# Optimization experiments

Measured on AMD Instinct MI355X. Metric: run time of the kernel, lower is better.

The kernel has to match this reference:

```python
import jax, jax.numpy as jnp
import numpy as np

B, C1, C2, H, W = 8, 256, 512, 56, 56

def setup_inputs() -> dict:
    key = jax.random.key(0)
    k1, k2, k3, k4, k5 = jax.random.split(key, 5)
    return {
        "x1": jax.random.normal(k1, (B, C1, H, W), dtype=jnp.float32),
        "x2": jax.random.normal(k2, (B, C2, H, W), dtype=jnp.float32),
        "W_proj": jax.random.normal(k3, (C1, C2), dtype=jnp.float32) * (1.0 / np.sqrt(C2)),
        "b_proj": jax.random.normal(k4, (C1,), dtype=jnp.float32) * 0.01,
        "gamma": jax.random.normal(k5, (1,), dtype=jnp.float32) * 0.1,
    }

def reference(x1, x2, W_proj, b_proj, gamma):
    b, c, h, w = x1.shape
    n = h * w
    # 1x1 conv projection C2 -> C1
    x2p = jnp.einsum('oc,bchw->bohw', W_proj, x2) + b_proj[None, :, None, None]
    query = x1.reshape(b, c, n).transpose(0, 2, 1)   # [B, N, C]
    key_ = x2p.reshape(b, c, n)                      # [B, C, N]
    value = x2p.reshape(b, c, n).transpose(0, 2, 1)  # [B, N, C]
    energy = jnp.einsum('bnc,bcm->bnm', query, key_)  # [B, N, N]
    # inverted-energy softmax: max - energy, then softmax over last dim
    energy_new = jnp.max(energy, axis=-1, keepdims=True) - energy
    attention = jax.nn.softmax(energy_new, axis=-1)
    out = jnp.einsum('bnm,bmc->bnc', attention, value)  # [B, N, C]
    out = out.transpose(0, 2, 1).reshape(b, c, h, w)
    return gamma[0] * out + x1
```

## Files before the change

kernel.cpp:

```cpp
#include <hip/hip_runtime.h>
#include <hip/hip_bf16.h>

#define C1 256
#define C2 512
#define NSP 3136
#define NT 98

typedef __attribute__((ext_vector_type(8))) short bf16x8;
typedef __attribute__((ext_vector_type(4))) float f32x4;

__device__ __forceinline__ ushort f2b(float f) {
  __hip_bfloat16 h = __float2bfloat16(f);
  return *reinterpret_cast<ushort*>(&h);
}
__device__ __forceinline__ float b2f(ushort u) {
  union { unsigned int i; float f; } v; v.i = ((unsigned int)u) << 16; return v.f;
}
__device__ __forceinline__ void gload16(const ushort* g, ushort* l) {
  __builtin_amdgcn_global_load_lds(
      (const __attribute__((address_space(1))) void*)g,
      (__attribute__((address_space(3))) void*)l, 16, 0, 0);
}
__device__ __forceinline__ void block_bar() {
  asm volatile("" ::: "memory");
  __builtin_amdgcn_s_barrier();
  asm volatile("" ::: "memory");
}

__global__ __launch_bounds__(256) void k_wtf(const float* __restrict__ W,
                                             ushort* __restrict__ Wf) {
  int ot = blockIdx.x;
  int tid = threadIdx.x;
  int lane = tid & 63, l15 = lane & 15, g = (lane >> 4) & 3;
  int cc0 = (tid >> 6) * 4;
  const float* src = W + (size_t)(ot * 16 + l15) * C2 + g * 8;
#pragma unroll
  for (int k = 0; k < 4; k++) {
    int cc = cc0 + k;
    float4 u0 = *reinterpret_cast<const float4*>(src + cc * 32);
    float4 u1 = *reinterpret_cast<const float4*>(src + cc * 32 + 4);
    bf16x8 v;
    v[0] = (short)f2b(u0.x); v[1] = (short)f2b(u0.y);
    v[2] = (short)f2b(u0.z); v[3] = (short)f2b(u0.w);
    v[4] = (short)f2b(u1.x); v[5] = (short)f2b(u1.y);
    v[6] = (short)f2b(u1.z); v[7] = (short)f2b(u1.w);
    *reinterpret_cast<bf16x8*>(Wf + ((size_t)(ot * 16 + cc)) * 512 + lane * 8) = v;
  }
}

__global__ __launch_bounds__(256) void k_x1t(const float* __restrict__ x1,
                                             ushort* __restrict__ x1t) {
  __shared__ float t[32][33];
  int b = blockIdx.z;
  int n0 = blockIdx.x * 32;
  int c0 = blockIdx.y * 32;
  int tid = threadIdx.x;
  int r = tid >> 3, q = (tid & 7) * 4;
  const float* src = x1 + ((size_t)b * C1 + (c0 + r)) * NSP + n0 + q;
  float4 v = *reinterpret_cast<const float4*>(src);
  t[r][q] = v.x; t[r][q + 1] = v.y; t[r][q + 2] = v.z; t[r][q + 3] = v.w;
  __syncthreads();
  ushort4 o;
  o.x = f2b(t[q + 0][r]); o.y = f2b(t[q + 1][r]);
  o.z = f2b(t[q + 2][r]); o.w = f2b(t[q + 3][r]);
  *reinterpret_cast<ushort4*>(x1t + ((size_t)b * NSP + n0 + r) * C1 + c0 + q) = o;
}

__global__ __launch_bounds__(256) void k_x2f(const float* __restrict__ x2,
                                             ushort* __restrict__ x2f) {
  __shared__ float t[32][33];
  int b = blockIdx.z;
  int n0 = blockIdx.x * 32;
  int cc = blockIdx.y;
  int c0 = cc * 32;
  int tid = threadIdx.x;
  int r = tid >> 3, q = (tid & 7) * 4;
  const float* src = x2 + ((size_t)b * C2 + (c0 + r)) * NSP + n0 + q;
  float4 v = *reinterpret_cast<const float4*>(src);
  t[r][q] = v.x; t[r][q + 1] = v.y; t[r][q + 2] = v.z; t[r][q + 3] = v.w;
  __syncthreads();
  int l15 = tid & 15, g = (tid >> 4) & 3, sub = tid >> 6;
  int ntl = sub & 1, ih = sub >> 1;
  int nl = ntl * 16 + l15;
  int cl = g * 8 + ih * 4;
  ushort4 o;
  o.x = f2b(t[cl + 0][nl]); o.y = f2b(t[cl + 1][nl]);
  o.z = f2b(t[cl + 2][nl]); o.w = f2b(t[cl + 3][nl]);
  int nt16 = (n0 >> 4) + ntl;
  *reinterpret_cast<ushort4*>(
      x2f + (((size_t)b * 196 + nt16) * 16 + cc) * 512 + (size_t)(tid & 63) * 8 + ih * 4) = o;
}

__global__ __launch_bounds__(256) void k_proj(const ushort* __restrict__ Wf,
    const ushort* __restrict__ x2f, const float* __restrict__ bias,
    ushort* __restrict__ Kf, ushort* __restrict__ Vf) {
  __shared__ __align__(16) ushort WL[2][8][512];
  __shared__ __align__(16) ushort XL[2][4][512];
  int bid = blockIdx.x;
  int b = bid & 7;
  int tq = bid >> 3;
  int oh = tq & 1;
  int nt = tq >> 1;
  int tid = threadIdx.x;
  int w = tid >> 6, lane = tid & 63, l15 = lane & 15, g = lane >> 4;
  int wq = w >> 1, wn = w & 1;
  int ot0 = oh * 8;
  int nt0 = nt * 4;

  auto stage = [&](int buf, int cc) {
#pragma unroll
    for (int j = 0; j < 3; j++) {
      int chunk = w * 3 + j;
      if (chunk < 8) {
        gload16(Wf + ((size_t)(ot0 + chunk) * 16 + cc) * 512 + lane * 8,
                &WL[buf][chunk][0]);
      } else {
        gload16(x2f + (((size_t)b * 196 + nt0 + (chunk - 8)) * 16 + cc) * 512 + lane * 8,
                &XL[buf][chunk - 8][0]);
      }
    }
  };

  f32x4 zero = {0.f, 0.f, 0.f, 0.f};
  f32x4 acc[4][2];
#pragma unroll
  for (int a = 0; a < 4; a++)
#pragma unroll
    for (int v = 0; v < 2; v++) acc[a][v] = zero;

  stage(0, 0);
  __syncthreads();

  for (int cc = 0; cc < 16; ++cc) {
    int cur = cc & 1;
    if (cc < 15) stage(cur ^ 1, cc + 1);
    bf16x8 A[4], Bf[2];
#pragma unroll
    for (int a = 0; a < 4; a++)
      A[a] = *reinterpret_cast<const bf16x8*>(&WL[cur][wq * 4 + a][lane * 8]);
#pragma unroll
    for (int v = 0; v < 2; v++)
      Bf[v] = *reinterpret_cast<const bf16x8*>(&XL[cur][wn * 2 + v][lane * 8]);
#pragma unroll
    for (int a = 0; a < 4; a++)
#pragma unroll
      for (int v = 0; v < 2; v++)
        acc[a][v] = __builtin_amdgcn_mfma_f32_16x16x32_bf16(A[a], Bf[v], acc[a][v], 0, 0, 0);
    __syncthreads();
  }

  int obase = oh * 128 + wq * 64;
  float4 bias4[4];
#pragma unroll
  for (int a = 0; a < 4; a++)
    bias4[a] = *reinterpret_cast<const float4*>(&bias[obase + a * 16 + g * 4]);

  int gk = (g & 1) * 4;
#pragma unroll
  for (int a = 0; a < 4; a++) {
    int laneK = (((2 * a + (g >> 1)) & 3) << 4) | l15;
    size_t oK = (size_t)(oh * 4 + wq * 2 + (a >> 1));
#pragma unroll
    for (int v = 0; v < 2; v++) {
      int nK = nt * 4 + wn * 2 + v;
      ushort4 st;
      st.x = f2b(acc[a][v][0] + bias4[a].x);
      st.y = f2b(acc[a][v][1] + bias4[a].y);
      st.z = f2b(acc[a][v][2] + bias4[a].z);
      st.w = f2b(acc[a][v][3] + bias4[a].w);
      *reinterpret_cast<ushort4*>(
          Kf + ((((size_t)b * 196 + nK) * 8 + oK) * 64 + laneK) * 8 + gk) = st;
    }
  }
  int nV = nt * 2 + wn;
#pragma unroll
  for (int v = 0; v < 2; v++) {
    int gv = ((v * 2 + (l15 >> 3)) & 3) << 4;
    int iV = l15 & 7;
#pragma unroll
    for (int a = 0; a < 4; a++) {
      int cs = oh * 8 + wq * 4 + a;
      size_t basev = ((((size_t)b * 98 + nV) * 16 + cs) * 64 + gv) * 8 + iV;
      const float* bp4 = reinterpret_cast<const float*>(&bias4[a]);
#pragma unroll
      for (int r = 0; r < 4; r++)
        Vf[basev + (size_t)(g * 4 + r) * 8] = f2b(acc[a][v][r] + bp4[r]);
    }
  }
}

template<int SPLIT>
__global__ __launch_bounds__(256, 3) void k_attn(
    const ushort* __restrict__ x1t, const ushort* __restrict__ Kf,
    const ushort* __restrict__ Vf, const float* __restrict__ x1,
    const float* __restrict__ gamma, float* __restrict__ out,
    ushort* __restrict__ Po, float* __restrict__ Mv, float* __restrict__ Lv) {
  __shared__ __align__(16) ushort Kt[2][8192];
  __shared__ __align__(16) ushort Vt[8192];
  __shared__ __align__(16) ushort Plds[4][16][36];
  int bid = blockIdx.x;
  int b = bid & 7;
  int qt = SPLIT ? (bid >> 4) : (bid >> 3);
  int h = SPLIT ? ((bid >> 3) & 1) : 0;
  int t0 = h * 49;
  int t1 = SPLIT ? (t0 + 49) : NT;
  int tid = threadIdx.x;
  int w = tid >> 6;
  int lane = tid & 63;
  int l15 = lane & 15;
  int g = lane >> 4;
  int n0 = qt * 64 + w * 16;

  bf16x8 qf[8];
  const ushort* qb = x1t + ((size_t)b * NSP + n0 + l15) * C1 + g * 8;
#pragma unroll
  for (int cc = 0; cc < 8; cc++)
    qf[cc] = *reinterpret_cast<const bf16x8*>(qb + cc * 32);

  f32x4 zero = {0.f, 0.f, 0.f, 0.f};
  f32x4 O[16];
#pragma unroll
  for (int i = 0; i < 16; i++) O[i] = zero;
  f32x4 O17 = zero;
  float M[4];
#pragma unroll
  for (int r = 0; r < 4; r++) M[r] = -3.0e38f;
  bf16x8 onesf;
#pragma unroll
  for (int i = 0; i < 8; i++) onesf[i] = (short)0x3F80;

  const ushort* kg = Kf + (size_t)b * 196 * 8 * 512;
  const ushort* vg = Vf + (size_t)b * 98 * 16 * 512;
  int soff = w * 2048;

  {
    const ushort* ks = kg + (size_t)t0 * 8192 + soff + lane * 8;
#pragma unroll
    for (int j = 0; j < 4; ++j) gload16(ks + j * 512, &Kt[0][soff] + j * 512);
  }
  asm volatile("s_waitcnt vmcnt(0)" ::: "memory");
  block_bar();

  int cur = 0;
  for (int t = t0; t < t1; ++t) {
    {
      const ushort* vs = vg + (size_t)t * 8192 + soff + lane * 8;
#pragma unroll
      for (int j = 0; j < 4; ++j) gload16(vs + j * 512, &Vt[soff] + j * 512);
    }
    asm volatile("" ::: "memory");
    if (t + 1 < t1) {
      const ushort* ks = kg + (size_t)(t + 1) * 8192 + soff + lane * 8;
#pragma unroll
      for (int j = 0; j < 4; ++j) gload16(ks + j * 512, &Kt[cur ^ 1][soff] + j * 512);
    }
    asm volatile("" ::: "memory");

    f32x4 s0a = zero, s0b = zero, s1a = zero, s1b = zero;
    const ushort* kb = &Kt[cur][0];
    __builtin_amdgcn_s_setprio(1);
#pragma unroll
    for (int cc = 0; cc < 8; cc += 2) {
      bf16x8 k00 = *reinterpret_cast<const bf16x8*>(kb + ((size_t)cc * 64 + lane) * 8);
      bf16x8 k10 = *reinterpret_cast<const bf16x8*>(kb + ((size_t)(8 + cc) * 64 + lane) * 8);
      bf16x8 k01 = *reinterpret_cast<const bf16x8*>(kb + ((size_t)(cc + 1) * 64 + lane) * 8);
      bf16x8 k11 = *reinterpret_cast<const bf16x8*>(kb + ((size_t)(9 + cc) * 64 + lane) * 8);
      s0a = __builtin_amdgcn_mfma_f32_16x16x32_bf16(qf[cc], k00, s0a, 0, 0, 0);
      s1a = __builtin_amdgcn_mfma_f32_16x16x32_bf16(qf[cc], k10, s1a, 0, 0, 0);
      s0b = __builtin_amdgcn_mfma_f32_16x16x32_bf16(qf[cc + 1], k01, s0b, 0, 0, 0);
      s1b = __builtin_amdgcn_mfma_f32_16x16x32_bf16(qf[cc + 1], k11, s1b, 0, 0, 0);
    }
    __builtin_amdgcn_s_setprio(0);

    float a0[4], a1[4], tmax[4];
#pragma unroll
    for (int r = 0; r < 4; r++) {
      a0[r] = -(s0a[r] + s0b[r]);
      a1[r] = -(s1a[r] + s1b[r]);
      float mx = fmaxf(a0[r], a1[r]);
      mx = fmaxf(mx, __shfl_xor(mx, 1));
      mx = fmaxf(mx, __shfl_xor(mx, 2));
      mx = fmaxf(mx, __shfl_xor(mx, 4));
      mx = fmaxf(mx, __shfl_xor(mx, 8));
      tmax[r] = mx;
    }
    float d01 = fmaxf(tmax[0] - M[0], tmax[1] - M[1]);
    float d23 = fmaxf(tmax[2] - M[2], tmax[3] - M[3]);
    if (__any(fmaxf(d01, d23) > 3.0f)) {
      float scv[4];
#pragma unroll
      for (int r = 0; r < 4; r++) {
        float nm = fmaxf(M[r], tmax[r]);
        scv[r] = __expf(M[r] - nm);
        M[r] = nm;
      }
#pragma unroll
      for (int i = 0; i < 16; i++) {
#pragma unroll
        for (int r = 0; r < 4; r++) O[i][r] *= scv[r];
      }
#pragma unroll
      for (int r = 0; r < 4; r++) O17[r] *= scv[r];
    }
#pragma unroll
    for (int r = 0; r < 4; r++) {
      float p0 = __expf(a0[r] - M[r]);
      float p1 = __expf(a1[r] - M[r]);
      Plds[w][g * 4 + r][l15] = f2b(p0);
      Plds[w][g * 4 + r][16 + l15] = f2b(p1);
    }

    if (t + 1 < t1) { asm volatile("s_waitcnt vmcnt(4)" ::: "memory"); }
    else            { asm volatile("s_waitcnt vmcnt(0)" ::: "memory"); }
    block_bar();

    bf16x8 pf = *reinterpret_cast<const bf16x8*>(&Plds[w][l15][g * 8]);
    __builtin_amdgcn_s_setprio(1);
#pragma unroll
    for (int cs = 0; cs < 16; ++cs) {
      bf16x8 vf = *reinterpret_cast<const bf16x8*>(&Vt[0] + ((size_t)cs * 64 + lane) * 8);
      O[cs] = __builtin_amdgcn_mfma_f32_16x16x32_bf16(pf, vf, O[cs], 0, 0, 0);
    }
    O17 = __builtin_amdgcn_mfma_f32_16x16x32_bf16(pf, onesf, O17, 0, 0, 0);
    __builtin_amdgcn_s_setprio(0);

    asm volatile("s_waitcnt vmcnt(0)" ::: "memory");
    block_bar();
    cur ^= 1;
  }

  if (SPLIT) {
    int pb = bid;
    int nloc = w * 16 + g * 4;
#pragma unroll
    for (int cs = 0; cs < 16; cs++) {
      int c = cs * 16 + l15;
      ushort4 st;
      st.x = f2b(O[cs][0]); st.y = f2b(O[cs][1]);
      st.z = f2b(O[cs][2]); st.w = f2b(O[cs][3]);
      *reinterpret_cast<ushort4*>(Po + ((size_t)pb * 256 + c) * 64 + nloc) = st;
    }
    if (l15 == 0) {
#pragma unroll
      for (int r = 0; r < 4; r++) {
        Mv[(size_t)pb * 64 + nloc + r] = M[r];
        Lv[(size_t)pb * 64 + nloc + r] = O17[r];
      }
    }
  } else {
    float gm = gamma[0];
    float rl[4];
#pragma unroll
    for (int r = 0; r < 4; r++) rl[r] = gm / O17[r];
    size_t ob = (size_t)b * C1 * NSP + n0 + (size_t)g * 4;
#pragma unroll
    for (int cs = 0; cs < 16; cs++) {
      size_t idx = ob + (size_t)(cs * 16 + l15) * NSP;
      float4 x4 = *reinterpret_cast<const float4*>(&x1[idx]);
      float4 o4;
      o4.x = O[cs][0] * rl[0] + x4.x;
      o4.y = O[cs][1] * rl[1] + x4.y;
      o4.z = O[cs][2] * rl[2] + x4.z;
      o4.w = O[cs][3] * rl[3] + x4.w;
      *reinterpret_cast<float4*>(&out[idx]) = o4;
    }
  }
}

__global__ __launch_bounds__(256) void k_comb(
    const ushort* __restrict__ Po, const float* __restrict__ Mv,
    const float* __restrict__ Lv, const float* __restrict__ x1,
    const float* __restrict__ gamma, float* __restrict__ out) {
  int bid = blockIdx.x;
  int b = bid & 7;
  int qt = bid >> 3;
  int tid = threadIdx.x;
  int n = tid & 63;
  int c0 = (tid >> 6) * 64;
  int pb0 = qt * 16 + b;
  int pb1 = qt * 16 + 8 + b;
  int n0 = qt * 64;
  float M0 = Mv[(size_t)pb0 * 64 + n], M1 = Mv[(size_t)pb1 * 64 + n];
  float L0 = Lv[(size_t)pb0 * 64 + n], L1 = Lv[(size_t)pb1 * 64 + n];
  float Ms = fmaxf(M0, M1);
  float w0 = __expf(M0 - Ms), w1 = __expf(M1 - Ms);
  float rl = gamma[0] / (w0 * L0 + w1 * L1);
  const ushort* p0 = Po + (size_t)pb0 * 16384 + n;
  const ushort* p1 = Po + (size_t)pb1 * 16384 + n;
#pragma unroll 4
  for (int c = c0; c < c0 + 64; ++c) {
    float o0 = b2f(p0[(size_t)c * 64]);
    float o1 = b2f(p1[(size_t)c * 64]);
    size_t idx = ((size_t)b * C1 + c) * NSP + n0 + n;
    out[idx] = (w0 * o0 + w1 * o1) * rl + x1[idx];
  }
}

extern "C" void kernel_launch(void* const* d_in, const int* in_sizes, int n_in,
                              void* d_out, int out_size, void* d_ws, size_t ws_size,
                              hipStream_t stream) {
  const float* x1 = (const float*)d_in[0];
  const float* x2 = (const float*)d_in[1];
  const float* W = (const float*)d_in[2];
  const float* bp = (const float*)d_in[3];
  const float* gamma = (const float*)d_in[4];
  float* out = (float*)d_out;

  char* ws = (char*)d_ws;
  ushort* Wf = (ushort*)(ws + 0);
  ushort* x1t = (ushort*)(ws + 524288);
  ushort* Kf = (ushort*)(ws + 13369344);
  ushort* Vf = (ushort*)(ws + 26214400);
  ushort* Po = (ushort*)(ws + 39059456);
  float* Mv = (float*)(ws + 64749568);
  float* Lv = (float*)(ws + 64950272);
  ushort* x2f = (ushort*)d_out;

  k_wtf<<<dim3(16), dim3(256), 0, stream>>>(W, Wf);
  k_x1t<<<dim3(98, 8, 8), dim3(256), 0, stream>>>(x1, x1t);
  k_x2f<<<dim3(98, 16, 8), dim3(256), 0, stream>>>(x2, x2f);
  k_proj<<<dim3(784), dim3(256), 0, stream>>>(Wf, x2f, bp, Kf, Vf);

  if (ws_size >= 65150976ULL) {
    k_attn<1><<<dim3(784), dim3(256), 0, stream>>>(x1t, Kf, Vf, x1, gamma, out,
                                                   Po, Mv, Lv);
    k_comb<<<dim3(392), dim3(256), 0, stream>>>(Po, Mv, Lv, x1, gamma, out);
  } else {
    k_attn<0><<<dim3(392), dim3(256), 0, stream>>>(x1t, Kf, Vf, x1, gamma, out,
                                                   Po, Mv, Lv);
  }
}
```

Baseline: 255.6 us.

## Add stream-K cooperative attention kernel with in-kernel grid-sync combine

Adds a cooperative attention kernel that splits the 8x49 query-tile by 98 key-tile work evenly across 768 blocks (51 tiles each, stream-K style). Each block crosses query-tile boundaries, spilling partial O/M/L for tiles it does not own, then does a grid-wide sync and the owning block merges the partials and writes the output. This removes the separate combine kernel launch and the load imbalance of fixed 784/392-block splits. In exchange it needs cooperative launch with all 768 blocks co-resident, and it falls back to the old path if that launch fails. It also shrinks the workspace offsets and adds an lgkmcnt wait before reading P from LDS.

```diff
diff --git a/kernel.cpp b/kernel.cpp
--- a/kernel.cpp
+++ b/kernel.cpp
@@ -1,5 +1,8 @@
 #include <hip/hip_runtime.h>
 #include <hip/hip_bf16.h>
+#include <hip/hip_cooperative_groups.h>
+
+namespace cg = cooperative_groups;
 
 #define C1 256
 #define C2 512
@@ -189,6 +192,256 @@
   }
 }
 
+__global__ __launch_bounds__(256, 3) void k_attn_q(
+    const ushort* __restrict__ x1t, const ushort* __restrict__ Kf,
+    const ushort* __restrict__ Vf, const float* __restrict__ x1,
+    const float* __restrict__ gamma, float* __restrict__ out,
+    ushort* __restrict__ Po, float* __restrict__ Mv, float* __restrict__ Lv) {
+  __shared__ __align__(16) ushort Kt[2][8192];
+  __shared__ __align__(16) ushort Vt[8192];
+  __shared__ __align__(16) ushort Plds[4][16][36];
+  int bid = blockIdx.x;
+  int x = bid & 7;
+  int j = bid >> 3;
+  int s = 51 * j; if (s > 4802) s = 4802;
+  int e = 51 * j + 51; if (e > 4802) e = 4802;
+  int tid = threadIdx.x;
+  int w = tid >> 6;
+  int lane = tid & 63;
+  int l15 = lane & 15;
+  int g = lane >> 4;
+  int nloc = w * 16 + g * 4;
+
+  const ushort* kg = Kf + (size_t)x * 196 * 8 * 512;
+  const ushort* vg = Vf + (size_t)x * 98 * 16 * 512;
+  int soff = w * 2048;
+
+  f32x4 zero = {0.f, 0.f, 0.f, 0.f};
+  f32x4 O[16];
+  f32x4 O17 = zero;
+  float M[4];
+  bf16x8 qf[8];
+  bf16x8 onesf;
+#pragma unroll
+  for (int i = 0; i < 8; i++) onesf[i] = (short)0x3F80;
+
+  auto resetacc = [&]() {
+#pragma unroll
+    for (int i = 0; i < 16; i++) O[i] = zero;
+    O17 = zero;
+#pragma unroll
+    for (int r = 0; r < 4; r++) M[r] = -3.0e38f;
+  };
+  auto loadQ = [&](int u) {
+    const ushort* qb = x1t + ((size_t)x * NSP + u * 64 + w * 16 + l15) * C1 + g * 8;
+#pragma unroll
+    for (int cc = 0; cc < 8; cc++)
+      qf[cc] = *reinterpret_cast<const bf16x8*>(qb + cc * 32);
+  };
+
+  int u = 0;
+  if (s < e) {
+    u = s / 98;
+    loadQ(u);
+    resetacc();
+    int kv0 = s - u * 98;
+    {
+      const ushort* ks = kg + (size_t)kv0 * 8192 + soff + lane * 8;
+#pragma unroll
+      for (int jj = 0; jj < 4; ++jj) gload16(ks + jj * 512, &Kt[0][soff] + jj * 512);
+    }
+    asm volatile("s_waitcnt vmcnt(0)" ::: "memory");
+    block_bar();
+
+    int cur = 0;
+    int kv = kv0;
+    for (int i = s; i < e; ++i) {
+      {
+        const ushort* vs = vg + (size_t)kv * 8192 + soff + lane * 8;
+#pragma unroll
+        for (int jj = 0; jj < 4; ++jj) gload16(vs + jj * 512, &Vt[soff] + jj * 512);
+      }
+      asm volatile("" ::: "memory");
+      if (i + 1 < e) {
+        int kvn = (kv + 1 == 98) ? 0 : kv + 1;
+        const ushort* ks = kg + (size_t)kvn * 8192 + soff + lane * 8;
+#pragma unroll
+        for (int jj = 0; jj < 4; ++jj) gload16(ks + jj * 512, &Kt[cur ^ 1][soff] + jj * 512);
+      }
+      asm volatile("" ::: "memory");
+
+      f32x4 s0a = zero, s0b = zero, s1a = zero, s1b = zero;
+      const ushort* kb = &Kt[cur][0];
+      __builtin_amdgcn_s_setprio(1);
+#pragma unroll
+      for (int cc = 0; cc < 8; cc += 2) {
+        bf16x8 k00 = *reinterpret_cast<const bf16x8*>(kb + ((size_t)cc * 64 + lane) * 8);
+        bf16x8 k10 = *reinterpret_cast<const bf16x8*>(kb + ((size_t)(8 + cc) * 64 + lane) * 8);
+        bf16x8 k01 = *reinterpret_cast<const bf16x8*>(kb + ((size_t)(cc + 1) * 64 + lane) * 8);
+        bf16x8 k11 = *reinterpret_cast<const bf16x8*>(kb + ((size_t)(9 + cc) * 64 + lane) * 8);
+        s0a = __builtin_amdgcn_mfma_f32_16x16x32_bf16(qf[cc], k00, s0a, 0, 0, 0);
+        s1a = __builtin_amdgcn_mfma_f32_16x16x32_bf16(qf[cc], k10, s1a, 0, 0, 0);
+        s0b = __builtin_amdgcn_mfma_f32_16x16x32_bf16(qf[cc + 1], k01, s0b, 0, 0, 0);
+        s1b = __builtin_amdgcn_mfma_f32_16x16x32_bf16(qf[cc + 1], k11, s1b, 0, 0, 0);
+      }
+      __builtin_amdgcn_s_setprio(0);
+
+      float a0[4], a1[4], tmax[4];
+#pragma unroll
+      for (int r = 0; r < 4; r++) {
+        a0[r] = -(s0a[r] + s0b[r]);
+        a1[r] = -(s1a[r] + s1b[r]);
+        float mx = fmaxf(a0[r], a1[r]);
+        mx = fmaxf(mx, __shfl_xor(mx, 1));
+        mx = fmaxf(mx, __shfl_xor(mx, 2));
+        mx = fmaxf(mx, __shfl_xor(mx, 4));
+        mx = fmaxf(mx, __shfl_xor(mx, 8));
+        tmax[r] = mx;
+      }
+      float d01 = fmaxf(tmax[0] - M[0], tmax[1] - M[1]);
+      float d23 = fmaxf(tmax[2] - M[2], tmax[3] - M[3]);
+      if (__any(fmaxf(d01, d23) > 3.0f)) {
+        float scv[4];
+#pragma unroll
+        for (int r = 0; r < 4; r++) {
+          float nm = fmaxf(M[r], tmax[r]);
+          scv[r] = __expf(M[r] - nm);
+          M[r] = nm;
+        }
+#pragma unroll
+        for (int i2 = 0; i2 < 16; i2++) {
+#pragma unroll
+          for (int r = 0; r < 4; r++) O[i2][r] *= scv[r];
+        }
+#pragma unroll
+        for (int r = 0; r < 4; r++) O17[r] *= scv[r];
+      }
+#pragma unroll
+      for (int r = 0; r < 4; r++) {
+        float p0 = __expf(a0[r] - M[r]);
+        float p1 = __expf(a1[r] - M[r]);
+        Plds[w][g * 4 + r][l15] = f2b(p0);
+        Plds[w][g * 4 + r][16 + l15] = f2b(p1);
+      }
+
+      if (i + 1 < e) { asm volatile("s_waitcnt vmcnt(4)" ::: "memory"); }
+      else           { asm volatile("s_waitcnt vmcnt(0)" ::: "memory"); }
+      block_bar();
+
+      asm volatile("s_waitcnt lgkmcnt(0)" ::: "memory");
+      bf16x8 pf = *reinterpret_cast<const bf16x8*>(&Plds[w][l15][g * 8]);
+      __builtin_amdgcn_s_setprio(1);
+#pragma unroll
+      for (int cs = 0; cs < 16; ++cs) {
+        bf16x8 vf = *reinterpret_cast<const bf16x8*>(&Vt[0] + ((size_t)cs * 64 + lane) * 8);
+        O[cs] = __builtin_amdgcn_mfma_f32_16x16x32_bf16(pf, vf, O[cs], 0, 0, 0);
+      }
+      O17 = __builtin_amdgcn_mfma_f32_16x16x32_bf16(pf, onesf, O17, 0, 0, 0);
+      __builtin_amdgcn_s_setprio(0);
+
+      asm volatile("s_waitcnt vmcnt(0)" ::: "memory");
+      block_bar();
+      cur ^= 1;
+
+      bool pend = (i + 1 == e) || (kv == 97);
+      if (pend) {
+        int owner = (u < 48) ? (98 * u + 47) / 51 : 94;
+        bool keep = (i + 1 == e) && (j == owner);
+        if (!keep) {
+          int firstj = (98 * u) / 51;
+          int k = j - firstj;
+          int ok = owner - firstj;
+          int slot = (x * 49 + u) * 2 + (k - (k > ok ? 1 : 0));
+#pragma unroll
+          for (int cs = 0; cs < 16; cs++) {
+            int c = cs * 16 + l15;
+            ushort4 st;
+            st.x = f2b(O[cs][0]); st.y = f2b(O[cs][1]);
+            st.z = f2b(O[cs][2]); st.w = f2b(O[cs][3]);
+            *reinterpret_cast<ushort4*>(Po + ((size_t)slot * 256 + c) * 64 + nloc) = st;
+          }
+          if (l15 == 0) {
+#pragma unroll
+            for (int r = 0; r < 4; r++) {
+              Mv[(size_t)slot * 64 + nloc + r] = M[r];
+              Lv[(size_t)slot * 64 + nloc + r] = O17[r];
+            }
+          }
+          if (i + 1 < e) { u += 1; loadQ(u); resetacc(); }
+        }
+      }
+      kv = (kv + 1 == 98) ? 0 : kv + 1;
+    }
+  }
+
+  __threadfence();
+  cg::this_grid().sync();
+  __threadfence();
+
+  if (s < e) {
+    int ul = (e - 1) / 98;
+    int owner = (ul < 48) ? (98 * ul + 47) / 51 : 94;
+    if (j == owner) {
+      int firstj = (98 * ul) / 51;
+      int lastj = (98 * ul + 97) / 51; if (lastj > 94) lastj = 94;
+      int np = lastj - firstj;
+      int base_u = (x * 49 + ul) * 2;
+      float Mg[4], wp[2][4], Lp[2][4], Mp[2][4];
+#pragma unroll
+      for (int r = 0; r < 4; r++) Mg[r] = M[r];
+      for (int p = 0; p < np; ++p) {
+#pragma unroll
+        for (int r = 0; r < 4; r++) {
+          Mp[p][r] = Mv[(size_t)(base_u + p) * 64 + nloc + r];
+          Lp[p][r] = Lv[(size_t)(base_u + p) * 64 + nloc + r];
+          Mg[r] = fmaxf(Mg[r], Mp[p][r]);
+        }
+      }
+      float wr[4], Lg[4];
+#pragma unroll
+      for (int r = 0; r < 4; r++) {
+        wr[r] = __expf(M[r] - Mg[r]);
+        Lg[r] = wr[r] * O17[r];
+      }
+      for (int p = 0; p < np; ++p) {
+#pragma unroll
+        for (int r = 0; r < 4; r++) {
+          wp[p][r] = __expf(Mp[p][r] - Mg[r]);
+          Lg[r] += wp[p][r] * Lp[p][r];
+        }
+      }
+      float gm = gamma[0];
+      float rl[4];
+#pragma unroll
+      for (int r = 0; r < 4; r++) rl[r] = gm / Lg[r];
+      size_t ob = (size_t)x * C1 * NSP + ul * 64 + nloc;
+#pragma unroll
+      for (int cs = 0; cs < 16; cs++) {
+        int c = cs * 16 + l15;
+        size_t idx = ob + (size_t)c * NSP;
+        float4 x4 = *reinterpret_cast<const float4*>(&x1[idx]);
+        float acc[4];
+#pragma unroll
+        for (int r = 0; r < 4; r++) acc[r] = wr[r] * O[cs][r];
+        for (int p = 0; p < np; ++p) {
+          const ushort* pp = Po + ((size_t)(base_u + p) * 256 + c) * 64 + nloc;
+          ushort4 pv = *reinterpret_cast<const ushort4*>(pp);
+          acc[0] += wp[p][0] * b2f(pv.x);
+          acc[1] += wp[p][1] * b2f(pv.y);
+          acc[2] += wp[p][2] * b2f(pv.z);
+          acc[3] += wp[p][3] * b2f(pv.w);
+        }
+        float4 o4;
+        o4.x = acc[0] * rl[0] + x4.x;
+        o4.y = acc[1] * rl[1] + x4.y;
+        o4.z = acc[2] * rl[2] + x4.z;
+        o4.w = acc[3] * rl[3] + x4.w;
+        *reinterpret_cast<float4*>(&out[idx]) = o4;
+      }
+    }
+  }
+}
+
 template<int SPLIT>
 __global__ __launch_bounds__(256, 3) void k_attn(
     const ushort* __restrict__ x1t, const ushort* __restrict__ Kf,
@@ -236,7 +489,7 @@
   {
     const ushort* ks = kg + (size_t)t0 * 8192 + soff + lane * 8;
 #pragma unroll
-    for (int j = 0; j < 4; ++j) gload16(ks + j * 512, &Kt[0][soff] + j * 512);
+    for (int jj = 0; jj < 4; ++jj) gload16(ks + jj * 512, &Kt[0][soff] + jj * 512);
   }
   asm volatile("s_waitcnt vmcnt(0)" ::: "memory");
   block_bar();
@@ -246,13 +499,13 @@
     {
       const ushort* vs = vg + (size_t)t * 8192 + soff + lane * 8;
 #pragma unroll
-      for (int j = 0; j < 4; ++j) gload16(vs + j * 512, &Vt[soff] + j * 512);
+      for (int jj = 0; jj < 4; ++jj) gload16(vs + jj * 512, &Vt[soff] + jj * 512);
     }
     asm volatile("" ::: "memory");
     if (t + 1 < t1) {
       const ushort* ks = kg + (size_t)(t + 1) * 8192 + soff + lane * 8;
 #pragma unroll
-      for (int j = 0; j < 4; ++j) gload16(ks + j * 512, &Kt[cur ^ 1][soff] + j * 512);
+      for (int jj = 0; jj < 4; ++jj) gload16(ks + jj * 512, &Kt[cur ^ 1][soff] + jj * 512);
     }
     asm volatile("" ::: "memory");
 
@@ -314,6 +567,7 @@
     else            { asm volatile("s_waitcnt vmcnt(0)" ::: "memory"); }
     block_bar();
 
+    asm volatile("s_waitcnt lgkmcnt(0)" ::: "memory");
     bf16x8 pf = *reinterpret_cast<const bf16x8*>(&Plds[w][l15][g * 8]);
     __builtin_amdgcn_s_setprio(1);
 #pragma unroll
@@ -408,12 +662,12 @@
 
   char* ws = (char*)d_ws;
   ushort* Wf = (ushort*)(ws + 0);
-  ushort* x1t = (ushort*)(ws + 524288);
-  ushort* Kf = (ushort*)(ws + 13369344);
-  ushort* Vf = (ushort*)(ws + 26214400);
-  ushort* Po = (ushort*)(ws + 39059456);
-  float* Mv = (float*)(ws + 64749568);
-  float* Lv = (float*)(ws + 64950272);
+  ushort* x1t = (ushort*)(ws + 262144);
+  ushort* Kf = (ushort*)(ws + 13107200);
+  ushort* Vf = (ushort*)(ws + 25952256);
+  ushort* Po = (ushort*)(ws + 38797312);
+  float* Mv = (float*)(ws + 64487424);
+  float* Lv = (float*)(ws + 64688128);
   ushort* x2f = (ushort*)d_out;
 
   k_wtf<<<dim3(16), dim3(256), 0, stream>>>(W, Wf);
@@ -421,12 +675,28 @@
   k_x2f<<<dim3(98, 16, 8), dim3(256), 0, stream>>>(x2, x2f);
   k_proj<<<dim3(784), dim3(256), 0, stream>>>(Wf, x2f, bp, Kf, Vf);
 
-  if (ws_size >= 65150976ULL) {
-    k_attn<1><<<dim3(784), dim3(256), 0, stream>>>(x1t, Kf, Vf, x1, gamma, out,
-                                                   Po, Mv, Lv);
-    k_comb<<<dim3(392), dim3(256), 0, stream>>>(Po, Mv, Lv, x1, gamma, out);
-  } else {
-    k_attn<0><<<dim3(392), dim3(256), 0, stream>>>(x1t, Kf, Vf, x1, gamma, out,
-                                                   Po, Mv, Lv);
-  }
-}
+  bool done = false;
+  if (ws_size >= 64888832ULL) {
+    const ushort* a0 = x1t; const ushort* a1 = Kf; const ushort* a2 = Vf;
+    const float* a3 = x1; const float* a4 = gamma; float* a5 = out;
+    ushort* a6 = Po; float* a7 = Mv; float* a8 = Lv;
+    void* kargs[] = {&a0, &a1, &a2, &a3, &a4, &a5, &a6, &a7, &a8};
+    hipError_t rc = hipLaunchCooperativeKernel(
+        reinterpret_cast<void*>(k_attn_q), dim3(768), dim3(256), kargs, 0, stream);
+    if (rc == hipSuccess) {
+      done = true;
+    } else {
+      (void)hipGetLastError();
+    }
+  }
+  if (!done) {
+    if (ws_size >= 64888832ULL) {
+      k_attn<1><<<dim3(784), dim3(256), 0, stream>>>(x1t, Kf, Vf, x1, gamma, out,
+                                                     Po, Mv, Lv);
+      k_comb<<<dim3(392), dim3(256), 0, stream>>>(Po, Mv, Lv, x1, gamma, out);
+    } else {
+      k_attn<0><<<dim3(392), dim3(256), 0, stream>>>(x1t, Kf, Vf, x1, gamma, out,
+                                                     Po, Mv, Lv);
+    }
+  }
+}
```

New measurement: 436.4 us. +70.7%, slower.

## Stream-K style balanced attention split across 768 blocks with three-way combine

Applied to the files above, without the earlier changes.

Replaces the fixed two-way KV split (784 blocks) with a stream-K partition. Each of 96 workers per batch processes a contiguous range of the flattened (query tile, KV tile) iteration space, and a new combine kernel merges up to three partials per query tile. The two transpose/convert kernels are fused into one launch, and the online-softmax rescale threshold is loosened from 3 to 8. The aim is to balance work evenly across CUs (768 = 3 per CU at occupancy 3) and remove tail imbalance and a launch. In exchange it adds branchy tile switching and Q reloads mid-loop. The looser rescale threshold raises bf16/overflow risk in the P values, and the workspace layout was changed with the ws_size fallback removed.

```diff
diff --git a/kernel.cpp b/kernel.cpp
--- a/kernel.cpp
+++ b/kernel.cpp
@@ -48,47 +48,44 @@
   }
 }
 
-__global__ __launch_bounds__(256) void k_x1t(const float* __restrict__ x1,
-                                             ushort* __restrict__ x1t) {
+__global__ __launch_bounds__(256) void k_prep(const float* __restrict__ x1,
+                                              const float* __restrict__ x2,
+                                              ushort* __restrict__ x1t,
+                                              ushort* __restrict__ x2f) {
   __shared__ float t[32][33];
   int b = blockIdx.z;
   int n0 = blockIdx.x * 32;
-  int c0 = blockIdx.y * 32;
+  int y = blockIdx.y;
   int tid = threadIdx.x;
   int r = tid >> 3, q = (tid & 7) * 4;
-  const float* src = x1 + ((size_t)b * C1 + (c0 + r)) * NSP + n0 + q;
-  float4 v = *reinterpret_cast<const float4*>(src);
-  t[r][q] = v.x; t[r][q + 1] = v.y; t[r][q + 2] = v.z; t[r][q + 3] = v.w;
-  __syncthreads();
-  ushort4 o;
-  o.x = f2b(t[q + 0][r]); o.y = f2b(t[q + 1][r]);
-  o.z = f2b(t[q + 2][r]); o.w = f2b(t[q + 3][r]);
-  *reinterpret_cast<ushort4*>(x1t + ((size_t)b * NSP + n0 + r) * C1 + c0 + q) = o;
-}
-
-__global__ __launch_bounds__(256) void k_x2f(const float* __restrict__ x2,
-                                             ushort* __restrict__ x2f) {
-  __shared__ float t[32][33];
-  int b = blockIdx.z;
-  int n0 = blockIdx.x * 32;
-  int cc = blockIdx.y;
-  int c0 = cc * 32;
-  int tid = threadIdx.x;
-  int r = tid >> 3, q = (tid & 7) * 4;
-  const float* src = x2 + ((size_t)b * C2 + (c0 + r)) * NSP + n0 + q;
-  float4 v = *reinterpret_cast<const float4*>(src);
-  t[r][q] = v.x; t[r][q + 1] = v.y; t[r][q + 2] = v.z; t[r][q + 3] = v.w;
-  __syncthreads();
-  int l15 = tid & 15, g = (tid >> 4) & 3, sub = tid >> 6;
-  int ntl = sub & 1, ih = sub >> 1;
-  int nl = ntl * 16 + l15;
-  int cl = g * 8 + ih * 4;
-  ushort4 o;
-  o.x = f2b(t[cl + 0][nl]); o.y = f2b(t[cl + 1][nl]);
-  o.z = f2b(t[cl + 2][nl]); o.w = f2b(t[cl + 3][nl]);
-  int nt16 = (n0 >> 4) + ntl;
-  *reinterpret_cast<ushort4*>(
-      x2f + (((size_t)b * 196 + nt16) * 16 + cc) * 512 + (size_t)(tid & 63) * 8 + ih * 4) = o;
+  if (y < 8) {
+    int c0 = y * 32;
+    const float* src = x1 + ((size_t)b * C1 + (c0 + r)) * NSP + n0 + q;
+    float4 v = *reinterpret_cast<const float4*>(src);
+    t[r][q] = v.x; t[r][q + 1] = v.y; t[r][q + 2] = v.z; t[r][q + 3] = v.w;
+    __syncthreads();
+    ushort4 o;
+    o.x = f2b(t[q + 0][r]); o.y = f2b(t[q + 1][r]);
+    o.z = f2b(t[q + 2][r]); o.w = f2b(t[q + 3][r]);
+    *reinterpret_cast<ushort4*>(x1t + ((size_t)b * NSP + n0 + r) * C1 + c0 + q) = o;
+  } else {
+    int cc = y - 8;
+    int c0 = cc * 32;
+    const float* src = x2 + ((size_t)b * C2 + (c0 + r)) * NSP + n0 + q;
+    float4 v = *reinterpret_cast<const float4*>(src);
+    t[r][q] = v.x; t[r][q + 1] = v.y; t[r][q + 2] = v.z; t[r][q + 3] = v.w;
+    __syncthreads();
+    int l15 = tid & 15, g = (tid >> 4) & 3, sub = tid >> 6;
+    int ntl = sub & 1, ih = sub >> 1;
+    int nl = ntl * 16 + l15;
+    int cl = g * 8 + ih * 4;
+    ushort4 o;
+    o.x = f2b(t[cl + 0][nl]); o.y = f2b(t[cl + 1][nl]);
+    o.z = f2b(t[cl + 2][nl]); o.w = f2b(t[cl + 3][nl]);
+    int nt16 = (n0 >> 4) + ntl;
+    *reinterpret_cast<ushort4*>(
+        x2f + (((size_t)b * 196 + nt16) * 16 + cc) * 512 + (size_t)(tid & 63) * 8 + ih * 4) = o;
+  }
 }
 
 __global__ __launch_bounds__(256) void k_proj(const ushort* __restrict__ Wf,
@@ -189,70 +186,77 @@
   }
 }
 
-template<int SPLIT>
-__global__ __launch_bounds__(256, 3) void k_attn(
+__global__ __launch_bounds__(256, 3) void k_attn_s(
     const ushort* __restrict__ x1t, const ushort* __restrict__ Kf,
-    const ushort* __restrict__ Vf, const float* __restrict__ x1,
-    const float* __restrict__ gamma, float* __restrict__ out,
+    const ushort* __restrict__ Vf,
     ushort* __restrict__ Po, float* __restrict__ Mv, float* __restrict__ Lv) {
   __shared__ __align__(16) ushort Kt[2][8192];
   __shared__ __align__(16) ushort Vt[8192];
   __shared__ __align__(16) ushort Plds[4][16][36];
   int bid = blockIdx.x;
-  int b = bid & 7;
-  int qt = SPLIT ? (bid >> 4) : (bid >> 3);
-  int h = SPLIT ? ((bid >> 3) & 1) : 0;
-  int t0 = h * 49;
-  int t1 = SPLIT ? (t0 + 49) : NT;
+  int x = bid & 7;
+  int j = bid >> 3;
+  int s = (4802 * j) / 96;
+  int e = (4802 * (j + 1)) / 96;
   int tid = threadIdx.x;
   int w = tid >> 6;
   int lane = tid & 63;
   int l15 = lane & 15;
   int g = lane >> 4;
-  int n0 = qt * 64 + w * 16;
-
-  bf16x8 qf[8];
-  const ushort* qb = x1t + ((size_t)b * NSP + n0 + l15) * C1 + g * 8;
-#pragma unroll
-  for (int cc = 0; cc < 8; cc++)
-    qf[cc] = *reinterpret_cast<const bf16x8*>(qb + cc * 32);
+  int nloc = w * 16 + g * 4;
+
+  const ushort* kg = Kf + (size_t)x * 196 * 8 * 512;
+  const ushort* vg = Vf + (size_t)x * 98 * 16 * 512;
+  int soff = w * 2048;
 
   f32x4 zero = {0.f, 0.f, 0.f, 0.f};
   f32x4 O[16];
-#pragma unroll
-  for (int i = 0; i < 16; i++) O[i] = zero;
   f32x4 O17 = zero;
   float M[4];
-#pragma unroll
-  for (int r = 0; r < 4; r++) M[r] = -3.0e38f;
+  bf16x8 qf[8];
   bf16x8 onesf;
 #pragma unroll
   for (int i = 0; i < 8; i++) onesf[i] = (short)0x3F80;
 
-  const ushort* kg = Kf + (size_t)b * 196 * 8 * 512;
-  const ushort* vg = Vf + (size_t)b * 98 * 16 * 512;
-  int soff = w * 2048;
-
+  auto resetacc = [&]() {
+#pragma unroll
+    for (int i = 0; i < 16; i++) O[i] = zero;
+    O17 = zero;
+#pragma unroll
+    for (int r = 0; r < 4; r++) M[r] = -3.0e38f;
+  };
+  auto loadQ = [&](int u) {
+    const ushort* qb = x1t + ((size_t)x * NSP + u * 64 + w * 16 + l15) * C1 + g * 8;
+#pragma unroll
+    for (int cc = 0; cc < 8; cc++)
+      qf[cc] = *reinterpret_cast<const bf16x8*>(qb + cc * 32);
+  };
+
+  int u = s / 98;
+  int kv = s - u * 98;
+  loadQ(u);
+  resetacc();
   {
-    const ushort* ks = kg + (size_t)t0 * 8192 + soff + lane * 8;
-#pragma unroll
-    for (int j = 0; j < 4; ++j) gload16(ks + j * 512, &Kt[0][soff] + j * 512);
+    const ushort* ks = kg + (size_t)kv * 8192 + soff + lane * 8;
+#pragma unroll
+    for (int jj = 0; jj < 4; ++jj) gload16(ks + jj * 512, &Kt[0][soff] + jj * 512);
   }
   asm volatile("s_waitcnt vmcnt(0)" ::: "memory");
   block_bar();
 
   int cur = 0;
-  for (int t = t0; t < t1; ++t) {
+  for (int i = s; i < e; ++i) {
     {
-      const ushort* vs = vg + (size_t)t * 8192 + soff + lane * 8;
-#pragma unroll
-      for (int j = 0; j < 4; ++j) gload16(vs + j * 512, &Vt[soff] + j * 512);
+      const ushort* vs = vg + (size_t)kv * 8192 + soff + lane * 8;
+#pragma unroll
+      for (int jj = 0; jj < 4; ++jj) gload16(vs + jj * 512, &Vt[soff] + jj * 512);
     }
     asm volatile("" ::: "memory");
-    if (t + 1 < t1) {
-      const ushort* ks = kg + (size_t)(t + 1) * 8192 + soff + lane * 8;
-#pragma unroll
-      for (int j = 0; j < 4; ++j) gload16(ks + j * 512, &Kt[cur ^ 1][soff] + j * 512);
+    if (i + 1 < e) {
+      int kvn = (kv == 97) ? 0 : kv + 1;
+      const ushort* ks = kg + (size_t)kvn * 8192 + soff + lane * 8;
+#pragma unroll
+      for (int jj = 0; jj < 4; ++jj) gload16(ks + jj * 512, &Kt[cur ^ 1][soff] + jj * 512);
     }
     asm volatile("" ::: "memory");
 
@@ -286,7 +290,7 @@
     }
     float d01 = fmaxf(tmax[0] - M[0], tmax[1] - M[1]);
     float d23 = fmaxf(tmax[2] - M[2], tmax[3] - M[3]);
-    if (__any(fmaxf(d01, d23) > 3.0f)) {
+    if (__any(fmaxf(d01, d23) > 8.0f)) {
       float scv[4];
 #pragma unroll
       for (int r = 0; r < 4; r++) {
@@ -295,25 +299,24 @@
         M[r] = nm;
       }
 #pragma unroll
-      for (int i = 0; i < 16; i++) {
-#pragma unroll
-        for (int r = 0; r < 4; r++) O[i][r] *= scv[r];
+      for (int i2 = 0; i2 < 16; i2++) {
+#pragma unroll
+        for (int r = 0; r < 4; r++) O[i2][r] *= scv[r];
       }
 #pragma unroll
       for (int r = 0; r < 4; r++) O17[r] *= scv[r];
     }
 #pragma unroll
     for (int r = 0; r < 4; r++) {
-      float p0 = __expf(a0[r] - M[r]);
-      float p1 = __expf(a1[r] - M[r]);
-      Plds[w][g * 4 + r][l15] = f2b(p0);
-      Plds[w][g * 4 + r][16 + l15] = f2b(p1);
-    }
-
-    if (t + 1 < t1) { asm volatile("s_waitcnt vmcnt(4)" ::: "memory"); }
-    else            { asm volatile("s_waitcnt vmcnt(0)" ::: "memory"); }
+      Plds[w][g * 4 + r][l15] = f2b(__expf(a0[r] - M[r]));
+      Plds[w][g * 4 + r][16 + l15] = f2b(__expf(a1[r] - M[r]));
+    }
+
+    if (i + 1 < e) { asm volatile("s_waitcnt vmcnt(4)" ::: "memory"); }
+    else           { asm volatile("s_waitcnt vmcnt(0)" ::: "memory"); }
     block_bar();
 
+    asm volatile("s_waitcnt lgkmcnt(0)" ::: "memory");
     bf16x8 pf = *reinterpret_cast<const bf16x8*>(&Plds[w][l15][g * 8]);
     __builtin_amdgcn_s_setprio(1);
 #pragma unroll
@@ -327,72 +330,68 @@
     asm volatile("s_waitcnt vmcnt(0)" ::: "memory");
     block_bar();
     cur ^= 1;
-  }
-
-  if (SPLIT) {
-    int pb = bid;
-    int nloc = w * 16 + g * 4;
-#pragma unroll
-    for (int cs = 0; cs < 16; cs++) {
-      int c = cs * 16 + l15;
-      ushort4 st;
-      st.x = f2b(O[cs][0]); st.y = f2b(O[cs][1]);
-      st.z = f2b(O[cs][2]); st.w = f2b(O[cs][3]);
-      *reinterpret_cast<ushort4*>(Po + ((size_t)pb * 256 + c) * 64 + nloc) = st;
-    }
-    if (l15 == 0) {
-#pragma unroll
-      for (int r = 0; r < 4; r++) {
-        Mv[(size_t)pb * 64 + nloc + r] = M[r];
-        Lv[(size_t)pb * 64 + nloc + r] = O17[r];
+
+    if ((i + 1 == e) || (kv == 97)) {
+      int firstj = (9408 * u + 95) / 4802;
+      int slot = (x * 49 + u) * 3 + (j - firstj);
+#pragma unroll
+      for (int cs = 0; cs < 16; cs++) {
+        int c = cs * 16 + l15;
+        ushort4 st;
+        st.x = f2b(O[cs][0]); st.y = f2b(O[cs][1]);
+        st.z = f2b(O[cs][2]); st.w = f2b(O[cs][3]);
+        *reinterpret_cast<ushort4*>(Po + ((size_t)slot * 256 + c) * 64 + nloc) = st;
       }
-    }
-  } else {
-    float gm = gamma[0];
-    float rl[4];
-#pragma unroll
-    for (int r = 0; r < 4; r++) rl[r] = gm / O17[r];
-    size_t ob = (size_t)b * C1 * NSP + n0 + (size_t)g * 4;
-#pragma unroll
-    for (int cs = 0; cs < 16; cs++) {
-      size_t idx = ob + (size_t)(cs * 16 + l15) * NSP;
-      float4 x4 = *reinterpret_cast<const float4*>(&x1[idx]);
-      float4 o4;
-      o4.x = O[cs][0] * rl[0] + x4.x;
-      o4.y = O[cs][1] * rl[1] + x4.y;
-      o4.z = O[cs][2] * rl[2] + x4.z;
-      o4.w = O[cs][3] * rl[3] + x4.w;
-      *reinterpret_cast<float4*>(&out[idx]) = o4;
-    }
-  }
-}
-
-__global__ __launch_bounds__(256) void k_comb(
+      if (l15 == 0) {
+#pragma unroll
+        for (int r = 0; r < 4; r++) {
+          Mv[(size_t)slot * 64 + nloc + r] = M[r];
+          Lv[(size_t)slot * 64 + nloc + r] = O17[r];
+        }
+      }
+      if (i + 1 < e && kv == 97) { u += 1; loadQ(u); resetacc(); }
+    }
+    kv = (kv == 97) ? 0 : kv + 1;
+  }
+}
+
+__global__ __launch_bounds__(256) void k_comb3(
     const ushort* __restrict__ Po, const float* __restrict__ Mv,
     const float* __restrict__ Lv, const float* __restrict__ x1,
     const float* __restrict__ gamma, float* __restrict__ out) {
   int bid = blockIdx.x;
-  int b = bid & 7;
-  int qt = bid >> 3;
+  int x = bid & 7;
+  int u = bid >> 3;
   int tid = threadIdx.x;
   int n = tid & 63;
   int c0 = (tid >> 6) * 64;
-  int pb0 = qt * 16 + b;
-  int pb1 = qt * 16 + 8 + b;
-  int n0 = qt * 64;
-  float M0 = Mv[(size_t)pb0 * 64 + n], M1 = Mv[(size_t)pb1 * 64 + n];
-  float L0 = Lv[(size_t)pb0 * 64 + n], L1 = Lv[(size_t)pb1 * 64 + n];
-  float Ms = fmaxf(M0, M1);
-  float w0 = __expf(M0 - Ms), w1 = __expf(M1 - Ms);
-  float rl = gamma[0] / (w0 * L0 + w1 * L1);
-  const ushort* p0 = Po + (size_t)pb0 * 16384 + n;
-  const ushort* p1 = Po + (size_t)pb1 * 16384 + n;
+  int firstj = (9408 * u + 95) / 4802;
+  int lastj = (96 * (98 * u + 97) + 95) / 4802;
+  int np = lastj - firstj + 1;
+  size_t base = (size_t)(x * 49 + u) * 3;
+  bool has2 = (np >= 3);
+
+  float M0 = Mv[(base + 0) * 64 + n];
+  float M1 = Mv[(base + 1) * 64 + n];
+  float M2 = has2 ? Mv[(base + 2) * 64 + n] : -3.0e38f;
+  float L0 = Lv[(base + 0) * 64 + n];
+  float L1 = Lv[(base + 1) * 64 + n];
+  float L2 = has2 ? Lv[(base + 2) * 64 + n] : 0.f;
+  float Mg = fmaxf(fmaxf(M0, M1), M2);
+  float w0 = __expf(M0 - Mg), w1 = __expf(M1 - Mg);
+  float w2 = has2 ? __expf(M2 - Mg) : 0.f;
+  float rl = gamma[0] / (w0 * L0 + w1 * L1 + w2 * L2);
+
+  const ushort* p0 = Po + ((base + 0) * 256) * 64 + n;
+  const ushort* p1 = Po + ((base + 1) * 256) * 64 + n;
+  const ushort* p2 = Po + ((base + 2) * 256) * 64 + n;
+  size_t ob = (size_t)x * C1 * NSP + u * 64 + n;
 #pragma unroll 4
   for (int c = c0; c < c0 + 64; ++c) {
-    float o0 = b2f(p0[(size_t)c * 64]);
-    float o1 = b2f(p1[(size_t)c * 64]);
-    size_t idx = ((size_t)b * C1 + c) * NSP + n0 + n;
-    out[idx] = (w0 * o0 + w1 * o1) * rl + x1[idx];
+    float acc = w0 * b2f(p0[(size_t)c * 64]) + w1 * b2f(p1[(size_t)c * 64]);
+    if (has2) acc += w2 * b2f(p2[(size_t)c * 64]);
+    size_t idx = ob + (size_t)c * NSP;
+    out[idx] = acc * rl + x1[idx];
   }
 }
 
@@ -408,25 +407,17 @@
 
   char* ws = (char*)d_ws;
   ushort* Wf = (ushort*)(ws + 0);
-  ushort* x1t = (ushort*)(ws + 524288);
-  ushort* Kf = (ushort*)(ws + 13369344);
-  ushort* Vf = (ushort*)(ws + 26214400);
-  ushort* Po = (ushort*)(ws + 39059456);
-  float* Mv = (float*)(ws + 64749568);
-  float* Lv = (float*)(ws + 64950272);
+  ushort* x1t = (ushort*)(ws + 262144);
+  ushort* Kf = (ushort*)(ws + 13107200);
+  ushort* Vf = (ushort*)(ws + 25952256);
+  ushort* Po = (ushort*)(ws + 38797312);
+  float* Mv = (float*)(ws + 77332480);
+  float* Lv = (float*)(ws + 77633536);
   ushort* x2f = (ushort*)d_out;
 
   k_wtf<<<dim3(16), dim3(256), 0, stream>>>(W, Wf);
-  k_x1t<<<dim3(98, 8, 8), dim3(256), 0, stream>>>(x1, x1t);
-  k_x2f<<<dim3(98, 16, 8), dim3(256), 0, stream>>>(x2, x2f);
+  k_prep<<<dim3(98, 24, 8), dim3(256), 0, stream>>>(x1, x2, x1t, x2f);
   k_proj<<<dim3(784), dim3(256), 0, stream>>>(Wf, x2f, bp, Kf, Vf);
-
-  if (ws_size >= 65150976ULL) {
-    k_attn<1><<<dim3(784), dim3(256), 0, stream>>>(x1t, Kf, Vf, x1, gamma, out,
-                                                   Po, Mv, Lv);
-    k_comb<<<dim3(392), dim3(256), 0, stream>>>(Po, Mv, Lv, x1, gamma, out);
-  } else {
-    k_attn<0><<<dim3(392), dim3(256), 0, stream>>>(x1t, Kf, Vf, x1, gamma, out,
-                                                   Po, Mv, Lv);
-  }
-}
+  k_attn_s<<<dim3(768), dim3(256), 0, stream>>>(x1t, Kf, Vf, Po, Mv, Lv);
+  k_comb3<<<dim3(392), dim3(256), 0, stream>>>(Po, Mv, Lv, x1, gamma, out);
+}
```

Result: faster. 246.0 us (-3.8%).
